# Performance work log

Measured on AMD Instinct MI355X. Metric: run time of the kernel, lower is better.

The kernel has to match this reference:

```python
import jax, jax.numpy as jnp
import numpy as np

B, S, D, H = 4, 2048, 1024, 16
DH = D // H  # 64
EPS = 1e-5


def setup_inputs() -> dict:
    key = jax.random.key(0)
    ks = jax.random.split(key, 6)
    scale = 0.02
    return {
        "x": jax.random.normal(ks[0], (B, S, D), dtype=jnp.float32),
        "Wq": jax.random.normal(ks[1], (H, D, DH), dtype=jnp.float32) * scale,
        "Wk": jax.random.normal(ks[2], (H, D, DH), dtype=jnp.float32) * scale,
        "Wv": jax.random.normal(ks[3], (H, D, DH), dtype=jnp.float32) * scale,
        "Wo": jax.random.normal(ks[4], (D, D), dtype=jnp.float32) * scale,
        "bo": jnp.zeros((D,), dtype=jnp.float32),
        "gamma": jnp.ones((D,), dtype=jnp.float32),
        "beta": jnp.zeros((D,), dtype=jnp.float32),
    }


def reference(x, Wq, Wk, Wv, Wo, bo, gamma, beta):
    # Per-head projections, stacked across heads: [B,H,S,DH]
    q = jnp.einsum("bsd,hdk->bhsk", x, Wq)
    k = jnp.einsum("bsd,hdk->bhsk", x, Wk)
    v = jnp.einsum("bsd,hdk->bhsk", x, Wv)
    inv_scale = 1.0 / jnp.sqrt(jnp.float32(DH))  # key.size(-1) == head_dim
    scores = jnp.einsum("bhqk,bhsk->bhqs", q, k) * inv_scale  # [B,H,S,S]
    attn = jax.nn.softmax(scores, axis=-1)
    ctx = jnp.einsum("bhqs,bhsk->bhqk", attn, v)  # [B,H,S,DH]
    # concat heads -> [B,S,D]
    concat = jnp.transpose(ctx, (0, 2, 1, 3)).reshape(B, S, D)
    proj = concat @ Wo + bo  # fc_out (Wo stored as [in,out])
    added = proj + x  # residual add
    mu = jnp.mean(added, axis=-1, keepdims=True)
    var = jnp.mean(jnp.square(added - mu), axis=-1, keepdims=True)
    normed = (added - mu) * jax.lax.rsqrt(var + EPS)
    return normed * gamma + beta
```

## Files before the change

### kernel.cpp

```cpp
#include <hip/hip_runtime.h>
#include <hip/hip_bf16.h>
#include <stdint.h>

#define DEV __device__ __forceinline__

typedef short s16x8 __attribute__((ext_vector_type(8)));
typedef float f32x4 __attribute__((ext_vector_type(4)));
typedef int i32x4 __attribute__((ext_vector_type(4)));

DEV void async_load16(const void* g, void* l) {
  __builtin_amdgcn_global_load_lds((void __attribute__((address_space(1)))*)(g),
                                   (void __attribute__((address_space(3)))*)(l),
                                   16, 0, 0);
}

DEV unsigned pack_bf16x2(float a, float b) {
  __hip_bfloat162 h = __float22bfloat162_rn(make_float2(a, b));
  union { __hip_bfloat162 h2; unsigned u; } cv;
  cv.h2 = h;
  return cv.u;
}

__global__ __launch_bounds__(256) void cast_x_kernel(const float* __restrict__ in,
                                                     __hip_bfloat16* __restrict__ out, int n4) {
  int i = blockIdx.x * 256 + threadIdx.x;
  if (i >= n4) return;
  float4 v = ((const float4*)in)[i];
  alignas(8) __hip_bfloat16 t[4] = {__float2bfloat16(v.x), __float2bfloat16(v.y),
                                    __float2bfloat16(v.z), __float2bfloat16(v.w)};
  *(uint2*)(out + (size_t)i * 4) = *(const uint2*)t;
}

__global__ __launch_bounds__(256) void transpose_cast_kernel(const float* __restrict__ src,
                                                             __hip_bfloat16* __restrict__ dst,
                                                             int R, int C, float scale) {
  __shared__ float tile[64][65];
  const int r0 = blockIdx.x * 64, c0 = blockIdx.y * 64, bt = blockIdx.z;
  const int tc = threadIdx.x & 63, tr = threadIdx.x >> 6;
  const float* sp = src + (size_t)bt * R * C;
#pragma unroll
  for (int rr = 0; rr < 64; rr += 4)
    tile[tr + rr][tc] = sp[(size_t)(r0 + tr + rr) * C + c0 + tc];
  __syncthreads();
  __hip_bfloat16* dp = dst + (size_t)bt * R * C;
#pragma unroll
  for (int rr = 0; rr < 64; rr += 4) {
    int cc = tr + rr;
    dp[(size_t)(c0 + cc) * R + r0 + tc] = __float2bfloat16(tile[tc][cc] * scale);
  }
}

__global__ __launch_bounds__(256) void qkv_transpose_kernel(const float* __restrict__ Wq,
                                                            const float* __restrict__ Wk,
                                                            const float* __restrict__ Wv,
                                                            __hip_bfloat16* __restrict__ dst,
                                                            float qscale) {
  __shared__ float tile[64][65];
  const int z = blockIdx.z, which = z >> 4, bt = z & 15;
  const int r0 = blockIdx.x * 64;
  const int tc = threadIdx.x & 63, tr = threadIdx.x >> 6;
  const float* src = (which == 0) ? Wq : (which == 1) ? Wk : Wv;
  const float scale = (which == 0) ? qscale : 1.0f;
  const float* sp = src + (size_t)bt * 1024 * 64;
#pragma unroll
  for (int rr = 0; rr < 64; rr += 4)
    tile[tr + rr][tc] = sp[(size_t)(r0 + tr + rr) * 64 + tc];
  __syncthreads();
  __hip_bfloat16* dp = dst + (size_t)z * 1024 * 64;
#pragma unroll
  for (int rr = 0; rr < 64; rr += 4) {
    int cc = tr + rr;
    dp[(size_t)(cc)*1024 + r0 + tc] = __float2bfloat16(tile[tc][cc] * scale);
  }
}

template <int MODE>
__global__ __launch_bounds__(256) void gemm128(const __hip_bfloat16* __restrict__ A,
                                               const __hip_bfloat16* __restrict__ Bt,
                                               void* __restrict__ out0,
                                               void* __restrict__ out1,
                                               void* __restrict__ out2,
                                               const float* __restrict__ bias,
                                               const float* __restrict__ resid,
                                               int M, int N, int K) {
  __shared__ __hip_bfloat16 As[128 * 32];
  __shared__ __hip_bfloat16 Bs[128 * 32];
  const int tid = threadIdx.x;
  const int lane = tid & 63, w = tid >> 6;
  const int lr = lane & 15, lq = lane >> 4;
  const int wm = w >> 1, wn = w & 1;
  const int m0 = blockIdx.y * 128, n0 = blockIdx.x * 128;

  const f32x4 fz = {0.f, 0.f, 0.f, 0.f};
  f32x4 acc[4][4];
#pragma unroll
  for (int i = 0; i < 4; i++)
#pragma unroll
    for (int j = 0; j < 4; j++) acc[i][j] = fz;

  const int kiters = K >> 5;
  for (int kt = 0; kt < kiters; kt++) {
    __syncthreads();
#pragma unroll
    for (int r = 0; r < 2; r++) {
      const int c = r * 256 + tid;
      const int row = c >> 2, kc = c & 3;
      async_load16((const short*)A + (size_t)(m0 + row) * K + kt * 32 + kc * 8,
                   (char*)As + (r * 256 + (tid & 0xC0)) * 16);
      async_load16((const short*)Bt + (size_t)(n0 + row) * K + kt * 32 + kc * 8,
                   (char*)Bs + (r * 256 + (tid & 0xC0)) * 16);
    }
    __syncthreads();
    const short* Ap = (const short*)As;
    const short* Bp = (const short*)Bs;
    s16x8 av[4], bv[4];
#pragma unroll
    for (int i = 0; i < 4; i++)
      av[i] = *(const s16x8*)(Ap + (wm * 64 + i * 16 + lr) * 32 + lq * 8);
#pragma unroll
    for (int j = 0; j < 4; j++)
      bv[j] = *(const s16x8*)(Bp + (wn * 64 + j * 16 + lr) * 32 + lq * 8);
#pragma unroll
    for (int i = 0; i < 4; i++)
#pragma unroll
      for (int j = 0; j < 4; j++)
        acc[i][j] = __builtin_amdgcn_mfma_f32_16x16x32_bf16(av[i], bv[j], acc[i][j], 0, 0, 0);
  }

  if constexpr (MODE == 0) {
    if (n0 < 2048) {
      __hip_bfloat16* dst01 = (__hip_bfloat16*)((n0 < 1024) ? out0 : out1);
#pragma unroll
      for (int i = 0; i < 4; i++)
#pragma unroll
        for (int j = 0; j < 4; j++)
#pragma unroll
          for (int r = 0; r < 4; r++) {
            const int row = m0 + wm * 64 + i * 16 + lq * 4 + r;
            const int col = n0 + wn * 64 + j * 16 + lr;
            const int bb = row >> 11, s = row & 2047;
            const int colq = col & 1023;
            dst01[((((size_t)bb * 16 + (colq >> 6)) * 2048 + s) << 6) + (col & 63)] =
                __float2bfloat16(acc[i][j][r]);
          }
    } else {
#pragma unroll
      for (int i = 0; i < 4; i++)
#pragma unroll
        for (int j = 0; j < 4; j++) {
          const int row0 = m0 + wm * 64 + i * 16 + lq * 4;
          const int col = (n0 - 2048) + wn * 64 + j * 16 + lr;
          const int bb = row0 >> 11, s0 = row0 & 2047;
          alignas(8) __hip_bfloat16 t4[4] = {
              __float2bfloat16(acc[i][j][0]), __float2bfloat16(acc[i][j][1]),
              __float2bfloat16(acc[i][j][2]), __float2bfloat16(acc[i][j][3])};
          *(uint2*)((__hip_bfloat16*)out2 + (size_t)bb * 2097152 + (size_t)col * 2048 + s0) =
              *(const uint2*)t4;
        }
    }
  } else {
#pragma unroll
    for (int i = 0; i < 4; i++)
#pragma unroll
      for (int j = 0; j < 4; j++)
#pragma unroll
        for (int r = 0; r < 4; r++) {
          const int row = m0 + wm * 64 + i * 16 + lq * 4 + r;
          const int col = n0 + wn * 64 + j * 16 + lr;
          const size_t idx = (size_t)row * 1024 + col;
          ((float*)out0)[idx] = acc[i][j][r] + bias[col] + resid[idx];
        }
  }
}

__global__ __launch_bounds__(128, 2) void flash_kernel(const __hip_bfloat16* __restrict__ Qg,
                                                       const __hip_bfloat16* __restrict__ Kg,
                                                       const __hip_bfloat16* __restrict__ Vtg,
                                                       __hip_bfloat16* __restrict__ Og) {
  __shared__ alignas(16) char smem[33280];
  float* xch = (float*)smem;
  float* lx = (float*)(smem + 32768);
  const int tid = threadIdx.x;
  const int lane = tid & 63, w = tid >> 6;
  const int lr = lane & 15, lq = lane >> 4;
  const int hb = blockIdx.x, qt = blockIdx.y;
  const int h = hb >> 2, b = hb & 3;
  const size_t bh = (size_t)b * 16 + h;
  const short* Qbase = (const short*)Qg + (bh * 2048 + (size_t)qt * 64) * 64;
  const short* Kbh = (const short*)Kg + bh * 2048 * 64;
  const short* Vbh = (const short*)Vtg + bh * 64 * 2048;

  const int rbase = (lr >> 2) * 8 + (lr & 3);
  const int gk = lr & 7;

  s16x8 qb[4][2];
#pragma unroll
  for (int nt = 0; nt < 4; nt++)
#pragma unroll
    for (int ks = 0; ks < 2; ks++)
      qb[nt][ks] = *(const s16x8*)(Qbase + (nt * 16 + lr) * 64 + ks * 32 + lq * 8);

  const f32x4 fz = {0.f, 0.f, 0.f, 0.f};
  f32x4 o[4][4];
#pragma unroll
  for (int i = 0; i < 4; i++)
#pragma unroll
    for (int j = 0; j < 4; j++) o[i][j] = fz;
  float lsum[4] = {0.f, 0.f, 0.f, 0.f};

  auto stage = [&](int sel, int kb) {
    char* Kl = smem + sel * 16384;
    char* Vl = Kl + 8192;
    const short* Ksrc = Kbh + kb * 64 * 64;
#pragma unroll
    for (int r = 0; r < 4; r++) {
      int c = r * 128 + tid;
      int row = c >> 3, ck = c & 7;
      int g = (row & 3) | (((row >> 3) & 1) << 2);
      async_load16(Ksrc + row * 64 + (ck ^ g) * 8, Kl + (r * 128 + (tid & 64)) * 16);
    }
#pragma unroll
    for (int r = 0; r < 4; r++) {
      int c = r * 128 + tid;
      int row = c >> 3, ck = c & 7;
      async_load16(Vbh + (size_t)row * 2048 + kb * 64 + ((ck ^ (row & 7))) * 8,
                   Vl + (r * 128 + (tid & 64)) * 16);
    }
  };

  stage(0, 0);
  __syncthreads();

  for (int kb = 0; kb < 32; kb++) {
    const int cur = kb & 1;
    if (kb + 1 < 32) stage(cur ^ 1, kb + 1);

    const short* Kp = (const short*)(smem + cur * 16384);
    const short* Vp = (const short*)(smem + cur * 16384 + 8192);

    union { i32x4 i; s16x8 s; } pa[4];
#pragma unroll
    for (int mt = 0; mt < 2; mt++) {
      const int kvrow = w * 32 + mt * 4 + rbase;
      s16x8 kf0 = *(const s16x8*)(Kp + kvrow * 64 + (((0 * 4 + lq) ^ gk)) * 8);
      s16x8 kf1 = *(const s16x8*)(Kp + kvrow * 64 + (((1 * 4 + lq) ^ gk)) * 8);
#pragma unroll
      for (int nt = 0; nt < 4; nt++) {
        f32x4 st = fz;
        st = __builtin_amdgcn_mfma_f32_16x16x32_bf16(kf0, qb[nt][0], st, 0, 0, 0);
        st = __builtin_amdgcn_mfma_f32_16x16x32_bf16(kf1, qb[nt][1], st, 0, 0, 0);
        float e0 = __builtin_amdgcn_exp2f(st[0]);
        float e1 = __builtin_amdgcn_exp2f(st[1]);
        float e2 = __builtin_amdgcn_exp2f(st[2]);
        float e3 = __builtin_amdgcn_exp2f(st[3]);
        lsum[nt] += (e0 + e1) + (e2 + e3);
        pa[nt].i[mt * 2 + 0] = (int)pack_bf16x2(e0, e1);
        pa[nt].i[mt * 2 + 1] = (int)pack_bf16x2(e2, e3);
      }
    }
#pragma unroll
    for (int ndh = 0; ndh < 4; ndh++) {
      int vrow = ndh * 16 + lr;
      s16x8 vb = *(const s16x8*)(Vp + vrow * 64 + (((w * 4 + lq) ^ (vrow & 7))) * 8);
#pragma unroll
      for (int nt = 0; nt < 4; nt++)
        o[nt][ndh] = __builtin_amdgcn_mfma_f32_16x16x32_bf16(pa[nt].s, vb, o[nt][ndh], 0, 0, 0);
    }

    __syncthreads();
  }

#pragma unroll
  for (int nt = 0; nt < 4; nt++) {
    lsum[nt] += __shfl_xor(lsum[nt], 16);
    lsum[nt] += __shfl_xor(lsum[nt], 32);
  }

  __syncthreads();
  if (w == 0) {
#pragma unroll
    for (int j = 0; j < 2; j++) {
#pragma unroll
      for (int ndh = 0; ndh < 4; ndh++)
        *(f32x4*)(xch + 0 * 2048 + (j * 4 + ndh) * 256 + lane * 4) = o[2 + j][ndh];
      if (lq == 0) lx[0 * 32 + j * 16 + lr] = lsum[2 + j];
    }
  } else {
#pragma unroll
    for (int j = 0; j < 2; j++) {
#pragma unroll
      for (int ndh = 0; ndh < 4; ndh++)
        *(f32x4*)(xch + 1 * 2048 + (j * 4 + ndh) * 256 + lane * 4) = o[0 + j][ndh];
      if (lq == 0) lx[1 * 32 + j * 16 + lr] = lsum[0 + j];
    }
  }
  __syncthreads();
  if (w == 0) {
#pragma unroll
    for (int j = 0; j < 2; j++) {
#pragma unroll
      for (int ndh = 0; ndh < 4; ndh++)
        o[0 + j][ndh] += *(const f32x4*)(xch + 1 * 2048 + (j * 4 + ndh) * 256 + lane * 4);
      lsum[0 + j] += lx[1 * 32 + j * 16 + lr];
#pragma unroll
      for (int r = 0; r < 4; r++) {
        float lv = __shfl(lsum[0 + j], lq * 4 + r);
        float inv = __builtin_amdgcn_rcpf(lv);
        int rowg = qt * 64 + (0 + j) * 16 + lq * 4 + r;
#pragma unroll
        for (int ndh = 0; ndh < 4; ndh++)
          Og[((size_t)b * 2048 + rowg) * 1024 + h * 64 + ndh * 16 + lr] =
              __float2bfloat16(o[0 + j][ndh][r] * inv);
      }
    }
  } else {
#pragma unroll
    for (int j = 0; j < 2; j++) {
#pragma unroll
      for (int ndh = 0; ndh < 4; ndh++)
        o[2 + j][ndh] += *(const f32x4*)(xch + 0 * 2048 + (j * 4 + ndh) * 256 + lane * 4);
      lsum[2 + j] += lx[0 * 32 + j * 16 + lr];
#pragma unroll
      for (int r = 0; r < 4; r++) {
        float lv = __shfl(lsum[2 + j], lq * 4 + r);
        float inv = __builtin_amdgcn_rcpf(lv);
        int rowg = qt * 64 + (2 + j) * 16 + lq * 4 + r;
#pragma unroll
        for (int ndh = 0; ndh < 4; ndh++)
          Og[((size_t)b * 2048 + rowg) * 1024 + h * 64 + ndh * 16 + lr] =
              __float2bfloat16(o[2 + j][ndh][r] * inv);
      }
    }
  }
}

__global__ __launch_bounds__(256) void ln_kernel(const float* __restrict__ tmp,
                                                 const float* __restrict__ gamma,
                                                 const float* __restrict__ beta,
                                                 float* __restrict__ out) {
  const int row = blockIdx.x, tid = threadIdx.x;
  const int lane = tid & 63, w = tid >> 6;
  const float* rp = tmp + (size_t)row * 1024;
  float4 v = ((const float4*)rp)[tid];
  float s = v.x + v.y + v.z + v.w;
  float ss = v.x * v.x + v.y * v.y + v.z * v.z + v.w * v.w;
#pragma unroll
  for (int off = 32; off >= 1; off >>= 1) {
    s += __shfl_xor(s, off);
    ss += __shfl_xor(ss, off);
  }
  __shared__ float red[8];
  if (lane == 0) {
    red[w] = s;
    red[4 + w] = ss;
  }
  __syncthreads();
  s = red[0] + red[1] + red[2] + red[3];
  ss = red[4] + red[5] + red[6] + red[7];
  const float mu = s * (1.0f / 1024.0f);
  const float var = ss * (1.0f / 1024.0f) - mu * mu;
  const float rstd = rsqrtf(var + 1e-5f);
  float4 g = ((const float4*)gamma)[tid];
  float4 be = ((const float4*)beta)[tid];
  float4 ov;
  ov.x = (v.x - mu) * rstd * g.x + be.x;
  ov.y = (v.y - mu) * rstd * g.y + be.y;
  ov.z = (v.z - mu) * rstd * g.z + be.z;
  ov.w = (v.w - mu) * rstd * g.w + be.w;
  ((float4*)(out + (size_t)row * 1024))[tid] = ov;
}

extern "C" void kernel_launch(void* const* d_in, const int* in_sizes, int n_in,
                              void* d_out, int out_size, void* d_ws, size_t ws_size,
                              hipStream_t stream) {
  (void)in_sizes; (void)n_in; (void)out_size; (void)ws_size;
  const float* x = (const float*)d_in[0];
  const float* Wq = (const float*)d_in[1];
  const float* Wk = (const float*)d_in[2];
  const float* Wv = (const float*)d_in[3];
  const float* Wo = (const float*)d_in[4];
  const float* bo = (const float*)d_in[5];
  const float* gamma = (const float*)d_in[6];
  const float* beta = (const float*)d_in[7];
  float* out = (float*)d_out;
  char* ws = (char*)d_ws;

  __hip_bfloat16* xb = (__hip_bfloat16*)(ws + 0);
  __hip_bfloat16* wqkvT = (__hip_bfloat16*)(ws + 16777216);
  __hip_bfloat16* woT = (__hip_bfloat16*)(ws + 23068672);
  __hip_bfloat16* Q = (__hip_bfloat16*)(ws + 25165824);
  __hip_bfloat16* Kt = (__hip_bfloat16*)(ws + 41943040);
  __hip_bfloat16* Vt = (__hip_bfloat16*)(ws + 58720256);
  __hip_bfloat16* cc = (__hip_bfloat16*)(ws + 75497472);
  float* tmp = (float*)(ws + 25165824);

  cast_x_kernel<<<8192, 256, 0, stream>>>(x, xb, 2097152);
  qkv_transpose_kernel<<<dim3(16, 1, 48), 256, 0, stream>>>(Wq, Wk, Wv, wqkvT,
                                                            0.125f * 1.44269504088896f);
  transpose_cast_kernel<<<dim3(16, 16, 1), 256, 0, stream>>>(Wo, woT, 1024, 1024, 1.0f);

  gemm128<0><<<dim3(24, 64), 256, 0, stream>>>(xb, wqkvT, Q, Kt, Vt, nullptr, nullptr,
                                               8192, 3072, 1024);

  flash_kernel<<<dim3(64, 32), 128, 0, stream>>>(Q, Kt, Vt, cc);

  gemm128<2><<<dim3(8, 64), 256, 0, stream>>>(cc, woT, tmp, nullptr, nullptr, bo, x,
                                              8192, 1024, 1024);
  ln_kernel<<<8192, 256, 0, stream>>>(tmp, gamma, beta, out);
}
```

Baseline: 313.9 us.

## Compute softmax row sums with an MFMA against a ones vector

```diff
diff --git a/kernel.cpp b/kernel.cpp
--- a/kernel.cpp
+++ b/kernel.cpp
@@ -177,9 +177,8 @@
                                                        const __hip_bfloat16* __restrict__ Kg,
                                                        const __hip_bfloat16* __restrict__ Vtg,
                                                        __hip_bfloat16* __restrict__ Og) {
-  __shared__ alignas(16) char smem[33280];
+  __shared__ alignas(16) char smem[32768];
   float* xch = (float*)smem;
-  float* lx = (float*)(smem + 32768);
   const int tid = threadIdx.x;
   const int lane = tid & 63, w = tid >> 6;
   const int lr = lane & 15, lq = lane >> 4;
@@ -200,13 +199,19 @@
     for (int ks = 0; ks < 2; ks++)
       qb[nt][ks] = *(const s16x8*)(Qbase + (nt * 16 + lr) * 64 + ks * 32 + lq * 8);
 
+  s16x8 vones;
+#pragma unroll
+  for (int e = 0; e < 8; e++) vones[e] = (short)0x3F80;
+
   const f32x4 fz = {0.f, 0.f, 0.f, 0.f};
   f32x4 o[4][4];
-#pragma unroll
-  for (int i = 0; i < 4; i++)
+  f32x4 ol[4];
+#pragma unroll
+  for (int i = 0; i < 4; i++) {
+    ol[i] = fz;
 #pragma unroll
     for (int j = 0; j < 4; j++) o[i][j] = fz;
-  float lsum[4] = {0.f, 0.f, 0.f, 0.f};
+  }
 
   auto stage = [&](int sel, int kb) {
     char* Kl = smem + sel * 16384;
@@ -253,11 +258,14 @@
         float e1 = __builtin_amdgcn_exp2f(st[1]);
         float e2 = __builtin_amdgcn_exp2f(st[2]);
         float e3 = __builtin_amdgcn_exp2f(st[3]);
-        lsum[nt] += (e0 + e1) + (e2 + e3);
         pa[nt].i[mt * 2 + 0] = (int)pack_bf16x2(e0, e1);
         pa[nt].i[mt * 2 + 1] = (int)pack_bf16x2(e2, e3);
       }
     }
+    __builtin_amdgcn_s_setprio(1);
+#pragma unroll
+    for (int nt = 0; nt < 4; nt++)
+      ol[nt] = __builtin_amdgcn_mfma_f32_16x16x32_bf16(pa[nt].s, vones, ol[nt], 0, 0, 0);
 #pragma unroll
     for (int ndh = 0; ndh < 4; ndh++) {
       int vrow = ndh * 16 + lr;
@@ -266,32 +274,27 @@
       for (int nt = 0; nt < 4; nt++)
         o[nt][ndh] = __builtin_amdgcn_mfma_f32_16x16x32_bf16(pa[nt].s, vb, o[nt][ndh], 0, 0, 0);
     }
+    __builtin_amdgcn_s_setprio(0);
 
     __syncthreads();
   }
 
-#pragma unroll
-  for (int nt = 0; nt < 4; nt++) {
-    lsum[nt] += __shfl_xor(lsum[nt], 16);
-    lsum[nt] += __shfl_xor(lsum[nt], 32);
-  }
-
   __syncthreads();
   if (w == 0) {
 #pragma unroll
     for (int j = 0; j < 2; j++) {
 #pragma unroll
       for (int ndh = 0; ndh < 4; ndh++)
-        *(f32x4*)(xch + 0 * 2048 + (j * 4 + ndh) * 256 + lane * 4) = o[2 + j][ndh];
-      if (lq == 0) lx[0 * 32 + j * 16 + lr] = lsum[2 + j];
+        *(f32x4*)(xch + 0 * 2560 + (j * 4 + ndh) * 256 + lane * 4) = o[2 + j][ndh];
+      *(f32x4*)(xch + 0 * 2560 + 2048 + j * 256 + lane * 4) = ol[2 + j];
     }
   } else {
 #pragma unroll
     for (int j = 0; j < 2; j++) {
 #pragma unroll
       for (int ndh = 0; ndh < 4; ndh++)
-        *(f32x4*)(xch + 1 * 2048 + (j * 4 + ndh) * 256 + lane * 4) = o[0 + j][ndh];
-      if (lq == 0) lx[1 * 32 + j * 16 + lr] = lsum[0 + j];
+        *(f32x4*)(xch + 1 * 2560 + (j * 4 + ndh) * 256 + lane * 4) = o[0 + j][ndh];
+      *(f32x4*)(xch + 1 * 2560 + 2048 + j * 256 + lane * 4) = ol[0 + j];
     }
   }
   __syncthreads();
@@ -300,12 +303,11 @@
     for (int j = 0; j < 2; j++) {
 #pragma unroll
       for (int ndh = 0; ndh < 4; ndh++)
-        o[0 + j][ndh] += *(const f32x4*)(xch + 1 * 2048 + (j * 4 + ndh) * 256 + lane * 4);
-      lsum[0 + j] += lx[1 * 32 + j * 16 + lr];
+        o[0 + j][ndh] += *(const f32x4*)(xch + 1 * 2560 + (j * 4 + ndh) * 256 + lane * 4);
+      f32x4 lt = ol[0 + j] + *(const f32x4*)(xch + 1 * 2560 + 2048 + j * 256 + lane * 4);
 #pragma unroll
       for (int r = 0; r < 4; r++) {
-        float lv = __shfl(lsum[0 + j], lq * 4 + r);
-        float inv = __builtin_amdgcn_rcpf(lv);
+        float inv = __builtin_amdgcn_rcpf(lt[r]);
         int rowg = qt * 64 + (0 + j) * 16 + lq * 4 + r;
 #pragma unroll
         for (int ndh = 0; ndh < 4; ndh++)
@@ -318,12 +320,11 @@
     for (int j = 0; j < 2; j++) {
 #pragma unroll
       for (int ndh = 0; ndh < 4; ndh++)
-        o[2 + j][ndh] += *(const f32x4*)(xch + 0 * 2048 + (j * 4 + ndh) * 256 + lane * 4);
-      lsum[2 + j] += lx[0 * 32 + j * 16 + lr];
+        o[2 + j][ndh] += *(const f32x4*)(xch + 0 * 2560 + (j * 4 + ndh) * 256 + lane * 4);
+      f32x4 lt = ol[2 + j] + *(const f32x4*)(xch + 0 * 2560 + 2048 + j * 256 + lane * 4);
 #pragma unroll
       for (int r = 0; r < 4; r++) {
-        float lv = __shfl(lsum[2 + j], lq * 4 + r);
-        float inv = __builtin_amdgcn_rcpf(lv);
+        float inv = __builtin_amdgcn_rcpf(lt[r]);
         int rowg = qt * 64 + (2 + j) * 16 + lq * 4 + r;
 #pragma unroll
         for (int ndh = 0; ndh < 4; ndh++)
```

Result: no change. 309.1 us (-1.5%).
